# Performance work log

Measured on AMD Instinct MI355X. Metric: run time of the kernel, lower is better.

Reference implementation:

```python
import jax, jax.numpy as jnp
import numpy as np

B, N, T, H, F = 2, 1024, 12, 64, 1

def _diffuse(x, a):
    # x: (B,C,V), a: (B,W,V)  ->  (B,C,W)   (einsum 'ncvl,nwv->ncwl' with l=1)
    return jnp.einsum('bcv,bwv->bcw', x, a)

def _sconv(x, supports, order, include_self, W, b):
    feats = [x] if include_self else []
    for a in supports:
        x1 = _diffuse(x, a)
        feats.append(x1)
        for _ in range(order - 1):
            x1 = _diffuse(x1, a)
            feats.append(x1)
    z = jnp.concatenate(feats, axis=1)
    return jnp.einsum('bcn,oc->bon', z, W) + b[None, :, None]

def _lin(x, W, b):
    # Conv1d/Conv2d with kernel 1 == channel-wise linear
    return jnp.einsum('bcn,oc->bon', x, W) + b[None, :, None]

def setup_inputs():
    key = jax.random.key(0)
    ks = jax.random.split(key, 12)
    x = jax.random.normal(ks[0], (B, F, N, T), jnp.float32)
    mask = jax.random.randint(ks[1], (B, F, N, T), 0, 2, jnp.int32)
    adj = jax.random.uniform(ks[2], (2, B, N, N), jnp.float32)
    adj = adj / (adj.sum(-1, keepdims=True) + 1e-8)  # compute_support row-normalization
    cin_gate = 5 * (2 * F + H)  # (order*support_len+1)*(d_in+num_units) = 5*66
    s = 0.1
    Wr = s * jax.random.normal(ks[3], (H, cin_gate)); br = jnp.zeros((H,), jnp.float32)
    Wu = s * jax.random.normal(ks[4], (H, cin_gate)); bu = jnp.zeros((H,), jnp.float32)
    Wc = s * jax.random.normal(ks[5], (H, cin_gate)); bc = jnp.zeros((H,), jnp.float32)
    Wfs = s * jax.random.normal(ks[6], (F, H)); bfs = jnp.zeros((F,), jnp.float32)
    Wdin = s * jax.random.normal(ks[7], (H, 2 * F + H)); bdin = jnp.zeros((H,), jnp.float32)
    Wgc = s * jax.random.normal(ks[8], (H, 2 * H)); bgc = jnp.zeros((H,), jnp.float32)
    Wlout = s * jax.random.normal(ks[9], (H, 2 * H)); blout = jnp.zeros((H,), jnp.float32)
    Wro = s * jax.random.normal(ks[10], (F, 2 * H)); bro = jnp.zeros((F,), jnp.float32)
    prelu_a = 0.25 * jnp.ones((1,), jnp.float32)
    return dict(x=x, mask=mask, adj=adj, Wr=Wr, br=br, Wu=Wu, bu=bu, Wc=Wc, bc=bc,
                Wfs=Wfs, bfs=bfs, Wdin=Wdin, bdin=bdin, Wgc=Wgc, bgc=bgc,
                Wlout=Wlout, blout=blout, Wro=Wro, bro=bro, prelu_a=prelu_a)

def _gril(x, mask, adj, Wr, br, Wu, bu, Wc, bc, Wfs, bfs, Wdin, bdin,
          Wgc, bgc, Wlout, blout, Wro, bro, prelu_a):
    supports = [adj[0], adj[1]]
    h0 = jnp.zeros((x.shape[0], H, x.shape[2]), x.dtype)

    def step(h, inp):
        x_s, m_s = inp                  # (B,F,N), (B,F,N) int
        m_f = m_s.astype(x_s.dtype)
        m_b = m_s.astype(bool)
        # first stage prediction from hidden state
        xs1 = _lin(h, Wfs, bfs)
        x1 = jnp.where(m_b, x_s, xs1)
        # spatial decoder (order=1, no attention)
        x_in = _lin(jnp.concatenate([x1, m_f, h], axis=1), Wdin, bdin)
        out = _sconv(x_in, supports, 1, False, Wgc, bgc)
        out = _lin(jnp.concatenate([out, h], axis=1), Wlout, blout)
        out = jnp.where(out >= 0, out, prelu_a * out)   # PReLU
        repr_s = jnp.concatenate([out, h], axis=1)      # (B,2H,N)
        xs2 = _lin(repr_s, Wro, bro)
        x2 = jnp.where(m_b, x1, xs2)
        # GCGRU cell update (order=2 diffusion per gate)
        inp_c = jnp.concatenate([x2, m_f], axis=1)
        xh = jnp.concatenate([inp_c, h], axis=1)
        r = jax.nn.sigmoid(_sconv(xh, supports, 2, True, Wr, br))
        u = jax.nn.sigmoid(_sconv(xh, supports, 2, True, Wu, bu))
        xc = jnp.concatenate([inp_c, r * h], axis=1)
        c = jnp.tanh(_sconv(xc, supports, 2, True, Wc, bc))
        h_new = u * h + (1.0 - u) * c
        return h_new, (xs2, xs1, repr_s)

    xs = jnp.moveaxis(x, -1, 0)     # (T,B,F,N)
    ms = jnp.moveaxis(mask, -1, 0)
    _, (imps, preds, reprs) = jax.lax.scan(step, h0, (xs, ms))
    imputations = jnp.moveaxis(imps, 0, -1)       # (B,F,N,T)
    predictions = jnp.moveaxis(preds, 0, -1)      # (B,F,N,T)
    representations = jnp.moveaxis(reprs, 0, -1)  # (B,2H,N,T)
    return imputations, predictions, representations

def reference(x, mask, adj, Wr, br, Wu, bu, Wc, bc, Wfs, bfs, Wdin, bdin,
              Wgc, bgc, Wlout, blout, Wro, bro, prelu_a):
    return _gril(x, mask, adj, Wr, br, Wu, bu, Wc, bc, Wfs, bfs, Wdin, bdin,
                 Wgc, bgc, Wlout, blout, Wro, bro, prelu_a)
```

## Files before the change

### kernel.cpp

```cpp
#include <hip/hip_runtime.h>
#include <hip/hip_bf16.h>
#include <cstddef>

#define NN 1024
#define BB 2
#define TT 12
#define ZS 352

typedef __attribute__((ext_vector_type(8))) short short8;
typedef __attribute__((ext_vector_type(4))) short short4v;
typedef __attribute__((ext_vector_type(4))) float f32x4;
typedef __hip_bfloat16 bf16;

__device__ __forceinline__ float sigmoidf_(float v) { return 1.0f / (1.0f + expf(-v)); }
__device__ __forceinline__ short bf16s(float f) { bf16 h = __float2bfloat16(f); return *reinterpret_cast<short*>(&h); }

__device__ __forceinline__ float mapcol(const float* src, int c) {
    if (c < 64) return src[2 + c];
    if (c == 64) return src[0];
    if (c == 65) return src[1];
    if (c < 68 || c >= 340) return 0.f;
    const int d = c - 68, bk = d / 68, off = d % 68;
    if (off < 64) return src[66 + bk * 66 + 2 + off];
    if (off == 64) return src[66 + bk * 66];
    if (off == 65) return src[66 + bk * 66 + 1];
    return 0.f;
}

__global__ __launch_bounds__(256) void k_prep(
    const float* __restrict__ Wgc, const float* __restrict__ bgc,
    const float* __restrict__ Wdin, const float* __restrict__ bdin,
    const float* __restrict__ Wlout, const float* __restrict__ blout,
    const float* __restrict__ Wfs,
    const float* __restrict__ Wr, const float* __restrict__ Wu, const float* __restrict__ Wc,
    float* __restrict__ Wcomb, float* __restrict__ bcomb, float* __restrict__ blout2,
    bf16* __restrict__ Wpre, bf16* __restrict__ Wrub, bf16* __restrict__ Wcb)
{
    const int idx = blockIdx.x * 256 + threadIdx.x;
    if (idx < 8448) {
        const int o = idx / 66, k = idx % 66;
        const float* g = Wgc + (size_t)(o & 63) * 128 + (o >> 6) * 64;
        float a = 0.f;
#pragma unroll 8
        for (int c = 0; c < 64; ++c) a += g[c] * Wdin[c * 66 + k];
        Wcomb[idx] = a;
    } else if (idx < 8576) {
        const int o = idx - 8448;
        const float* g = Wgc + (size_t)(o & 63) * 128 + (o >> 6) * 64;
        float a = 0.f;
#pragma unroll 8
        for (int c = 0; c < 64; ++c) a += g[c] * bdin[c];
        bcomb[o] = a;
    } else if (idx < 8640) {
        const int oc = idx - 8576;
        float a = blout[oc];
#pragma unroll 8
        for (int j = 0; j < 64; ++j) a += Wlout[(size_t)oc * 128 + j] * bgc[j];
        blout2[oc] = a;
    } else if (idx < 17856) {
        const int j = idx - 8640, r = j >> 6, k = j & 63;
        float v = 0.f;
        if (r == 0) v = Wfs[k];
        else if (r <= 128) {
            const int o = r - 1;
            const float* g = Wgc + (size_t)(o & 63) * 128 + (o >> 6) * 64;
#pragma unroll 8
            for (int c = 0; c < 64; ++c) v += g[c] * Wdin[c * 66 + 2 + k];
        }
        Wpre[j] = __float2bfloat16(v);
    } else if (idx < 62912) {
        const int j = idx - 17856, r = j / 352, c = j % 352;
        const float* src = (r < 64) ? (Wr + (size_t)r * 330) : (Wu + (size_t)(r - 64) * 330);
        Wrub[j] = __float2bfloat16(mapcol(src, c));
    } else if (idx < 85440) {
        const int j = idx - 62912, r = j / 352, c = j % 352;
        Wcb[j] = __float2bfloat16(mapcol(Wc + (size_t)r * 330, c));
    }
}

__global__ __launch_bounds__(256) void k_cvtT(const float* __restrict__ adj,
                                              bf16* __restrict__ adjb, bf16* __restrict__ adjtb)
{
    const int sb = blockIdx.z;
    const int r0 = blockIdx.y * 64, c0 = blockIdx.x * 64;
    const float* A = adj + ((size_t)sb << 20);
    __shared__ short tile[64][72];
    const int tr = threadIdx.x >> 4, tc = (threadIdx.x & 15) * 4;
#pragma unroll
    for (int i = 0; i < 4; ++i) {
        const int r = tr + i * 16;
        float4 v = *reinterpret_cast<const float4*>(&A[(size_t)(r0 + r) * NN + c0 + tc]);
        short4v o = { bf16s(v.x), bf16s(v.y), bf16s(v.z), bf16s(v.w) };
        *reinterpret_cast<short4v*>(&adjb[((size_t)sb << 20) + (size_t)(r0 + r) * NN + c0 + tc]) = o;
        tile[r][tc + 0] = o.x; tile[r][tc + 1] = o.y; tile[r][tc + 2] = o.z; tile[r][tc + 3] = o.w;
    }
    __syncthreads();
#pragma unroll
    for (int i = 0; i < 4; ++i) {
        const int v = tr + i * 16;
        short4v o = { tile[tc + 0][v], tile[tc + 1][v], tile[tc + 2][v], tile[tc + 3][v] };
        *reinterpret_cast<short4v*>(&adjtb[((size_t)sb << 20) + (size_t)(c0 + v) * NN + r0 + tc]) = o;
    }
}

__global__ __launch_bounds__(256) void k_a2(const bf16* __restrict__ adjb,
                                            const bf16* __restrict__ adjtb,
                                            bf16* __restrict__ adj2b)
{
    const int sb = blockIdx.z;
    const int wave = threadIdx.x >> 6, lane = threadIdx.x & 63;
    const int lr = lane & 15, lq = lane >> 4;
    const int v0 = blockIdx.x * 64 + wave * 16;
    const int w0 = blockIdx.y * 64;
    const bf16* AT = adjtb + ((size_t)sb << 20) + (size_t)(v0 + lr) * NN + lq * 8;
    const bf16* Ar = adjb + ((size_t)sb << 20) + (size_t)(w0 + lr) * NN + lq * 8;
    f32x4 acc[4];
#pragma unroll
    for (int m = 0; m < 4; ++m) acc[m] = (f32x4){0.f, 0.f, 0.f, 0.f};
#pragma unroll 4
    for (int k0 = 0; k0 < NN; k0 += 32) {
        short8 bfr = *reinterpret_cast<const short8*>(AT + k0);
        short8 af[4];
#pragma unroll
        for (int m = 0; m < 4; ++m)
            af[m] = *reinterpret_cast<const short8*>(Ar + (size_t)m * 16 * NN + k0);
#pragma unroll
        for (int m = 0; m < 4; ++m)
            acc[m] = __builtin_amdgcn_mfma_f32_16x16x32_bf16(af[m], bfr, acc[m], 0, 0, 0);
    }
    bf16* D = adj2b + ((size_t)sb << 20);
#pragma unroll
    for (int m = 0; m < 4; ++m)
#pragma unroll
        for (int q = 0; q < 4; ++q)
            D[(size_t)(w0 + m * 16 + lq * 4 + q) * NN + v0 + lr] = __float2bfloat16(acc[m][q]);
}

__global__ __launch_bounds__(64) void k_pre(
    const bf16* __restrict__ Wpre, const bf16* __restrict__ zT,
    const float* __restrict__ Wcomb, const float* __restrict__ bcomb,
    const float* __restrict__ bfsp,
    const float* __restrict__ x, const int* __restrict__ mask,
    bf16* __restrict__ yb, float* __restrict__ x1b, float* __restrict__ pred, int t)
{
    const int lane = threadIdx.x & 63, lr = lane & 15, lq = lane >> 4;
    const int p = blockIdx.x * 16 + lr;
    const bf16* B = zT + (size_t)p * ZS;
    f32x4 acc[9];
#pragma unroll
    for (int m = 0; m < 9; ++m) acc[m] = (f32x4){0.f, 0.f, 0.f, 0.f};
#pragma unroll
    for (int ks = 0; ks < 2; ++ks) {
        short8 bfr = *reinterpret_cast<const short8*>(B + ks * 32 + lq * 8);
#pragma unroll
        for (int m = 0; m < 9; ++m) {
            short8 af = *reinterpret_cast<const short8*>(Wpre + (size_t)(m * 16 + lr) * 64 + ks * 32 + lq * 8);
            acc[m] = __builtin_amdgcn_mfma_f32_16x16x32_bf16(af, bfr, acc[m], 0, 0, 0);
        }
    }
    const int b = p >> 10, n = p & (NN - 1);
    const size_t xi = (size_t)p * TT + t;
    const float xs1v = acc[0][0] + bfsp[0];
    const float xs1 = __shfl(xs1v, lr);
    const int mi = mask[xi];
    const float mf = (float)mi;
    const float x1 = mi ? x[xi] : xs1;
    if (lq == 0) { pred[xi] = xs1; x1b[p] = x1; }
#pragma unroll
    for (int m = 0; m < 9; ++m)
#pragma unroll
        for (int q = 0; q < 4; ++q) {
            const int o = m * 16 + lq * 4 + q - 1;
            if (o >= 0 && o < 128) {
                const float val = acc[m][q] + Wcomb[o * 66] * x1 + Wcomb[o * 66 + 1] * mf + bcomb[o];
                yb[(size_t)(b * 128 + o) * NN + n] = __float2bfloat16(val);
            }
        }
}

__global__ __launch_bounds__(256) void k_difN(
    int mode, const bf16* __restrict__ adjb, const bf16* __restrict__ adj2b,
    const bf16* __restrict__ yb, const bf16* __restrict__ zb, const bf16* __restrict__ zcb,
    float* __restrict__ gcT, bf16* __restrict__ zT, bf16* __restrict__ zcT)
{
    const int combo = blockIdx.y;
    const int wave = threadIdx.x >> 6, lane = threadIdx.x & 63;
    const int lr = lane & 15, lq = lane >> 4;
    const int n0 = blockIdx.x * 32;

    int s, b, ord; const bf16* X; bool toGc = false;
    if (mode == 0 && combo < 4) {
        s = combo >> 1; b = combo & 1; ord = 0; toGc = true;
        X = yb + ((size_t)(b * 128 + s * 64)) * NN;
    } else {
        const int i = (mode == 0) ? combo - 4 : combo;
        b = i & 1; s = (i >> 1) & 1; ord = i >> 2;
        X = ((mode == 0) ? zb : zcb) + ((size_t)b * 66) * NN;
    }
    const int sb = s * 2 + b;
    const bf16* M = (ord ? adj2b : adjb) + ((size_t)sb << 20);
    const bf16* A = M + (size_t)(n0 + lr) * NN + lq * 8;
    const bf16* Xp = X + (size_t)lr * NN + lq * 8;

    f32x4 acc[2][4];
#pragma unroll
    for (int nt = 0; nt < 2; ++nt)
#pragma unroll
        for (int m = 0; m < 4; ++m) acc[nt][m] = (f32x4){0.f, 0.f, 0.f, 0.f};
    const int vbeg = wave * 256;
#pragma unroll 2
    for (int i = 0; i < 8; ++i) {
        const int v0 = vbeg + i * 32;
        short8 bfr[2], af[4];
#pragma unroll
        for (int nt = 0; nt < 2; ++nt)
            bfr[nt] = *reinterpret_cast<const short8*>(A + (size_t)nt * 16 * NN + v0);
#pragma unroll
        for (int m = 0; m < 4; ++m)
            af[m] = *reinterpret_cast<const short8*>(Xp + (size_t)m * 16 * NN + v0);
#pragma unroll
        for (int nt = 0; nt < 2; ++nt)
#pragma unroll
            for (int m = 0; m < 4; ++m)
                acc[nt][m] = __builtin_amdgcn_mfma_f32_16x16x32_bf16(af[m], bfr[nt], acc[nt][m], 0, 0, 0);
    }
    __shared__ f32x4 red[3][2][4][64];
    if (wave > 0) {
#pragma unroll
        for (int nt = 0; nt < 2; ++nt)
#pragma unroll
            for (int m = 0; m < 4; ++m) red[wave - 1][nt][m][lane] = acc[nt][m];
    }
    __syncthreads();
    if (wave == 0) {
#pragma unroll
        for (int nt = 0; nt < 2; ++nt) {
#pragma unroll
            for (int m = 0; m < 4; ++m)
                acc[nt][m] += red[0][nt][m][lane] + red[1][nt][m][lane] + red[2][nt][m][lane];
            const int p = b * NN + n0 + nt * 16 + lr;
            if (toGc) {
#pragma unroll
                for (int m = 0; m < 4; ++m)
                    *reinterpret_cast<f32x4*>(&gcT[(size_t)p * 128 + s * 64 + m * 16 + lq * 4]) = acc[nt][m];
            } else {
                bf16* dst = ((mode == 0) ? zT : zcT) + (size_t)p * ZS + 68 + (s * 2 + ord) * 68;
#pragma unroll
                for (int m = 0; m < 4; ++m) {
                    short4v o = { bf16s(acc[nt][m][0]), bf16s(acc[nt][m][1]),
                                  bf16s(acc[nt][m][2]), bf16s(acc[nt][m][3]) };
                    *reinterpret_cast<short4v*>(dst + m * 16 + lq * 4) = o;
                }
            }
        }
    }
}

__global__ __launch_bounds__(256) void k_dif2(
    const bf16* __restrict__ adjb, const bf16* __restrict__ adj2b,
    const bf16* __restrict__ zb, bf16* __restrict__ zT, bf16* __restrict__ zcT)
{
    const int i = blockIdx.y;
    const int b = i & 1, s = (i >> 1) & 1, ord = i >> 2;
    const int sb = s * 2 + b;
    const int wave = threadIdx.x >> 6, lane = threadIdx.x & 63;
    const int lr = lane & 15, lq = lane >> 4;
    const int n0 = blockIdx.x * 16;
    const bf16* M = (ord ? adj2b : adjb) + ((size_t)sb << 20);
    const bf16* A = M + (size_t)(n0 + lr) * NN + lq * 8;
    const bf16* Xp = zb + ((size_t)(b * 66 + 64) + lr) * NN + lq * 8;

    f32x4 acc = (f32x4){0.f, 0.f, 0.f, 0.f};
    const short8 zsh = {0, 0, 0, 0, 0, 0, 0, 0};
    const int vbeg = wave * 256;
#pragma unroll 4
    for (int i2 = 0; i2 < 8; ++i2) {
        const int v0 = vbeg + i2 * 32;
        short8 bfr = *reinterpret_cast<const short8*>(A + v0);
        short8 af = (lr < 2) ? *reinterpret_cast<const short8*>(Xp + v0) : zsh;
        acc = __builtin_amdgcn_mfma_f32_16x16x32_bf16(af, bfr, acc, 0, 0, 0);
    }
    __shared__ f32x4 red2[3][64];
    if (wave > 0) red2[wave - 1][lane] = acc;
    __syncthreads();
    if (wave == 0 && lq == 0) {
        acc += red2[0][lane] + red2[1][lane] + red2[2][lane];
        const int p = b * NN + n0 + lr;
        const size_t off = (size_t)p * ZS + 68 + (s * 2 + ord) * 68 + 64;
#pragma unroll
        for (int q = 0; q < 2; ++q) {
            const bf16 v = __float2bfloat16(acc[q]);
            zT[off + q] = v; zcT[off + q] = v;
        }
    }
}

__global__ __launch_bounds__(256) void k_stepB(
    const float* __restrict__ gcT, const float* __restrict__ hTf,
    const float* __restrict__ Wlout, const float* __restrict__ blout2,
    const float* __restrict__ prelu_a, const float* __restrict__ Wro,
    const float* __restrict__ bro, const float* __restrict__ x1b,
    const int* __restrict__ mask,
    float* __restrict__ imp, float* __restrict__ repr,
    bf16* __restrict__ zb, bf16* __restrict__ zcb,
    bf16* __restrict__ zT, bf16* __restrict__ zcT, int t)
{
    const int wv = threadIdx.x >> 6, lane = threadIdx.x & 63;
    const int p = blockIdx.x * 4 + wv;
    const int b = p >> 10, n = p & (NN - 1);
    __shared__ float gl[4][64], hl[4][64];
    const float g = gcT[(size_t)p * 128 + lane] + gcT[(size_t)p * 128 + 64 + lane];
    const float hv = hTf[(size_t)p * 64 + lane];
    gl[wv][lane] = g;
    hl[wv][lane] = hv;
    __syncthreads();
    const float* w = Wlout + (size_t)lane * 128;
    float a = 0.f;
#pragma unroll 8
    for (int j = 0; j < 64; ++j)
        a += w[j] * gl[wv][j] + w[64 + j] * hl[wv][j];
    float v = a + blout2[lane];
    v = (v >= 0.f) ? v : prelu_a[0] * v;
    repr[(((size_t)b * 128 + lane) * NN + n) * TT + t] = v;
    repr[(((size_t)b * 128 + 64 + lane) * NN + n) * TT + t] = hv;
    float s = Wro[lane] * v + Wro[64 + lane] * hv;
#pragma unroll
    for (int off = 32; off > 0; off >>= 1) s += __shfl_xor(s, off);
    if (lane == 0) {
        const float xs2 = s + bro[0];
        const size_t xi = (size_t)p * TT + t;
        imp[xi] = xs2;
        const int mi = mask[xi];
        const float x2 = mi ? x1b[p] : xs2;
        const bf16 x2b = __float2bfloat16(x2);
        const bf16 mb = __float2bfloat16((float)mi);
        zb[((size_t)b * 66 + 64) * NN + n] = x2b;
        zb[((size_t)b * 66 + 65) * NN + n] = mb;
        zcb[((size_t)b * 66 + 64) * NN + n] = x2b;
        zcb[((size_t)b * 66 + 65) * NN + n] = mb;
        zT[(size_t)p * ZS + 64] = x2b; zT[(size_t)p * ZS + 65] = mb;
        zcT[(size_t)p * ZS + 64] = x2b; zcT[(size_t)p * ZS + 65] = mb;
    }
}

__global__ __launch_bounds__(128) void k_gates(
    const bf16* __restrict__ Wrub, const bf16* __restrict__ zT,
    const float* __restrict__ br, const float* __restrict__ bu,
    const float* __restrict__ hTf,
    float* __restrict__ uT, bf16* __restrict__ zcb, bf16* __restrict__ zcT)
{
    const int wave = threadIdx.x >> 6, lane = threadIdx.x & 63;
    const int lr = lane & 15, lq = lane >> 4;
    const int p = blockIdx.x * 16 + lr;
    const bf16* B = zT + (size_t)p * ZS;
    const bf16* WA = Wrub + (size_t)wave * 64 * ZS;
    f32x4 acc[4];
#pragma unroll
    for (int m = 0; m < 4; ++m) acc[m] = (f32x4){0.f, 0.f, 0.f, 0.f};
#pragma unroll 2
    for (int ks = 0; ks < 11; ++ks) {
        short8 bfr = *reinterpret_cast<const short8*>(B + ks * 32 + lq * 8);
#pragma unroll
        for (int m = 0; m < 4; ++m) {
            short8 af = *reinterpret_cast<const short8*>(WA + (size_t)(m * 16 + lr) * ZS + ks * 32 + lq * 8);
            acc[m] = __builtin_amdgcn_mfma_f32_16x16x32_bf16(af, bfr, acc[m], 0, 0, 0);
        }
    }
    const int b = p >> 10, n = p & (NN - 1);
    if (wave == 0) {
#pragma unroll
        for (int m = 0; m < 4; ++m) {
            short4v rq;
#pragma unroll
            for (int q = 0; q < 4; ++q) {
                const int oc = m * 16 + lq * 4 + q;
                const float rv = sigmoidf_(acc[m][q] + br[oc]);
                const float rh = rv * hTf[(size_t)p * 64 + oc];
                rq[q] = bf16s(rh);
                zcb[((size_t)b * 66 + oc) * NN + n] = __float2bfloat16(rh);
            }
            *reinterpret_cast<short4v*>(&zcT[(size_t)p * ZS + m * 16 + lq * 4]) = rq;
        }
    } else {
#pragma unroll
        for (int m = 0; m < 4; ++m) {
            f32x4 uq;
#pragma unroll
            for (int q = 0; q < 4; ++q) {
                const int oc = m * 16 + lq * 4 + q;
                uq[q] = sigmoidf_(acc[m][q] + bu[oc]);
            }
            *reinterpret_cast<f32x4*>(&uT[(size_t)p * 64 + m * 16 + lq * 4]) = uq;
        }
    }
}

__global__ __launch_bounds__(128) void k_cellpre(
    const bf16* __restrict__ Wcb, const bf16* __restrict__ zcT,
    const float* __restrict__ bc, const float* __restrict__ uT,
    float* __restrict__ hTf, bf16* __restrict__ zT, bf16* __restrict__ zb,
    const bf16* __restrict__ Wpre, const float* __restrict__ Wcomb,
    const float* __restrict__ bcomb, const float* __restrict__ bfsp,
    const float* __restrict__ x, const int* __restrict__ mask,
    bf16* __restrict__ yb, float* __restrict__ x1b, float* __restrict__ pred, int tn)
{
    const int wave = threadIdx.x >> 6, lane = threadIdx.x & 63;
    const int lr = lane & 15, lq = lane >> 4;
    const int p = blockIdx.x * 16 + lr;
    const int b = p >> 10, n = p & (NN - 1);
    __shared__ short hsm[16][72];
    __shared__ float xs1s[16];

    {
        const bf16* B = zcT + (size_t)p * ZS;
        f32x4 acc[2];
#pragma unroll
        for (int mm = 0; mm < 2; ++mm) acc[mm] = (f32x4){0.f, 0.f, 0.f, 0.f};
#pragma unroll 2
        for (int ks = 0; ks < 11; ++ks) {
            short8 bfr = *reinterpret_cast<const short8*>(B + ks * 32 + lq * 8);
#pragma unroll
            for (int mm = 0; mm < 2; ++mm) {
                const int m = wave * 2 + mm;
                short8 af = *reinterpret_cast<const short8*>(Wcb + (size_t)(m * 16 + lr) * ZS + ks * 32 + lq * 8);
                acc[mm] = __builtin_amdgcn_mfma_f32_16x16x32_bf16(af, bfr, acc[mm], 0, 0, 0);
            }
        }
#pragma unroll
        for (int mm = 0; mm < 2; ++mm) {
            const int m = wave * 2 + mm;
            f32x4 hq;
            short4v hb;
#pragma unroll
            for (int q = 0; q < 4; ++q) {
                const int oc = m * 16 + lq * 4 + q;
                const float cv = tanhf(acc[mm][q] + bc[oc]);
                const float uv = uT[(size_t)p * 64 + oc];
                const float ho = hTf[(size_t)p * 64 + oc];
                const float hn = uv * ho + (1.f - uv) * cv;
                hq[q] = hn;
                hb[q] = bf16s(hn);
                zb[((size_t)b * 66 + oc) * NN + n] = __float2bfloat16(hn);
            }
            *reinterpret_cast<f32x4*>(&hTf[(size_t)p * 64 + m * 16 + lq * 4]) = hq;
            *reinterpret_cast<short4v*>(&zT[(size_t)p * ZS + m * 16 + lq * 4]) = hb;
            *reinterpret_cast<short4v*>(&hsm[lr][m * 16 + lq * 4]) = hb;
        }
    }
    __syncthreads();

    {
        const int MB = wave ? 4 : 5;
        f32x4 acc[5];
#pragma unroll
        for (int m = 0; m < 5; ++m) acc[m] = (f32x4){0.f, 0.f, 0.f, 0.f};
#pragma unroll
        for (int ks = 0; ks < 2; ++ks) {
            short8 bfr = *reinterpret_cast<const short8*>(&hsm[lr][ks * 32 + lq * 8]);
#pragma unroll
            for (int m = 0; m < 5; ++m) {
                if (m < MB) {
                    const int mm = wave ? 5 + m : m;
                    short8 af = *reinterpret_cast<const short8*>(Wpre + (size_t)(mm * 16 + lr) * 64 + ks * 32 + lq * 8);
                    acc[m] = __builtin_amdgcn_mfma_f32_16x16x32_bf16(af, bfr, acc[m], 0, 0, 0);
                }
            }
        }
        if (wave == 0 && lq == 0) xs1s[lr] = acc[0][0] + bfsp[0];
        __syncthreads();
        const float xs1 = xs1s[lr];
        const size_t xi = (size_t)p * TT + tn;
        const int mi = mask[xi];
        const float mf = (float)mi;
        const float x1 = mi ? x[xi] : xs1;
        if (wave == 0 && lq == 0) { pred[xi] = xs1; x1b[p] = x1; }
#pragma unroll
        for (int m = 0; m < 5; ++m) {
            if (m < MB) {
                const int mm = wave ? 5 + m : m;
#pragma unroll
                for (int q = 0; q < 4; ++q) {
                    const int o = mm * 16 + lq * 4 + q - 1;
                    if (o >= 0 && o < 128) {
                        const float val = acc[m][q] + Wcomb[o * 66] * x1 + Wcomb[o * 66 + 1] * mf + bcomb[o];
                        yb[(size_t)(b * 128 + o) * NN + n] = __float2bfloat16(val);
                    }
                }
            }
        }
    }
}

extern "C" void kernel_launch(void* const* d_in, const int* in_sizes, int n_in,
                              void* d_out, int out_size, void* d_ws, size_t ws_size,
                              hipStream_t stream)
{
    const float* x     = (const float*)d_in[0];
    const int*   mask  = (const int*)  d_in[1];
    const float* adj   = (const float*)d_in[2];
    const float* Wr    = (const float*)d_in[3];
    const float* br    = (const float*)d_in[4];
    const float* Wu    = (const float*)d_in[5];
    const float* bu    = (const float*)d_in[6];
    const float* Wc    = (const float*)d_in[7];
    const float* bc    = (const float*)d_in[8];
    const float* Wfs   = (const float*)d_in[9];
    const float* bfs   = (const float*)d_in[10];
    const float* Wdin  = (const float*)d_in[11];
    const float* bdin  = (const float*)d_in[12];
    const float* Wgc   = (const float*)d_in[13];
    const float* bgc   = (const float*)d_in[14];
    const float* Wlout = (const float*)d_in[15];
    const float* blout = (const float*)d_in[16];
    const float* Wro   = (const float*)d_in[17];
    const float* bro   = (const float*)d_in[18];
    const float* pa    = (const float*)d_in[19];

    float* ws = (float*)d_ws;
    float* Wcomb  = ws + 0;
    float* bcomb  = ws + 8448;
    float* blout2 = ws + 8576;
    float* x1b    = ws + 8640;
    float* gcT    = ws + 10688;
    float* uT     = ws + 272832;
    float* hTf    = ws + 403904;
    bf16* bfp   = (bf16*)(ws + 534976);
    bf16* zb    = bfp + 0;
    bf16* zcb   = bfp + 135168;
    bf16* zT    = bfp + 270336;
    bf16* zcT   = bfp + 991232;
    bf16* adjb  = bfp + 1712128;
    bf16* adjtb = bfp + 5906432;
    bf16* adj2b = bfp + 10100736;
    bf16* yb    = bfp + 14295040;
    bf16* Wpre  = bfp + 14557184;
    bf16* Wrub  = bfp + 14566400;
    bf16* Wcb   = bfp + 14611456;

    float* imp  = (float*)d_out;
    float* pred = imp + (size_t)BB * NN * TT;
    float* repr = imp + (size_t)2 * BB * NN * TT;

    hipMemsetAsync(hTf, 0, 131072 * 4 + (size_t)1712128 * 2, stream);
    hipLaunchKernelGGL(k_prep, dim3(334), dim3(256), 0, stream,
                       Wgc, bgc, Wdin, bdin, Wlout, blout, Wfs, Wr, Wu, Wc,
                       Wcomb, bcomb, blout2, Wpre, Wrub, Wcb);
    hipLaunchKernelGGL(k_cvtT, dim3(16, 16, 4), dim3(256), 0, stream, adj, adjb, adjtb);
    hipLaunchKernelGGL(k_a2, dim3(16, 16, 4), dim3(256), 0, stream, adjb, adjtb, adj2b);

    hipLaunchKernelGGL(k_pre, dim3(128), dim3(64), 0, stream,
                       Wpre, zT, Wcomb, bcomb, bfs, x, mask, yb, x1b, pred, 0);

    for (int t = 0; t < TT; ++t) {
        const int ncombo = (t < TT - 1) ? 12 : 4;
        hipLaunchKernelGGL(k_difN, dim3(32, ncombo), dim3(256), 0, stream,
                           0, adjb, adj2b, yb, zb, zcb, gcT, zT, zcT);
        hipLaunchKernelGGL(k_stepB, dim3(512), dim3(256), 0, stream,
                           gcT, hTf, Wlout, blout2, pa, Wro, bro, x1b, mask,
                           imp, repr, zb, zcb, zT, zcT, t);
        if (t < TT - 1) {
            hipLaunchKernelGGL(k_dif2, dim3(64, 8), dim3(256), 0, stream,
                               adjb, adj2b, zb, zT, zcT);
            hipLaunchKernelGGL(k_gates, dim3(128), dim3(128), 0, stream,
                               Wrub, zT, br, bu, hTf, uT, zcb, zcT);
            hipLaunchKernelGGL(k_difN, dim3(32, 8), dim3(256), 0, stream,
                               1, adjb, adj2b, yb, zb, zcb, gcT, zT, zcT);
            hipLaunchKernelGGL(k_cellpre, dim3(128), dim3(128), 0, stream,
                               Wcb, zcT, bc, uT, hTf, zT, zb,
                               Wpre, Wcomb, bcomb, bfs, x, mask, yb, x1b, pred, t + 1);
        }
    }
}
```

Baseline: 765.2 us.

## Fuse output-readout stage into graph-diffusion kernel and retile adjacency-square GEMM

```diff
diff --git a/kernel.cpp b/kernel.cpp
--- a/kernel.cpp
+++ b/kernel.cpp
@@ -34,7 +34,8 @@
     const float* __restrict__ Wfs,
     const float* __restrict__ Wr, const float* __restrict__ Wu, const float* __restrict__ Wc,
     float* __restrict__ Wcomb, float* __restrict__ bcomb, float* __restrict__ blout2,
-    bf16* __restrict__ Wpre, bf16* __restrict__ Wrub, bf16* __restrict__ Wcb)
+    bf16* __restrict__ Wpre, bf16* __restrict__ Wrub, bf16* __restrict__ Wcb,
+    bf16* __restrict__ Wlb)
 {
     const int idx = blockIdx.x * 256 + threadIdx.x;
     if (idx < 8448) {
@@ -75,6 +76,9 @@
     } else if (idx < 85440) {
         const int j = idx - 62912, r = j / 352, c = j % 352;
         Wcb[j] = __float2bfloat16(mapcol(Wc + (size_t)r * 330, c));
+    } else if (idx < 93632) {
+        const int j = idx - 85440;
+        Wlb[j] = __float2bfloat16(Wlout[j]);
     }
 }
 
@@ -110,30 +114,38 @@
     const int sb = blockIdx.z;
     const int wave = threadIdx.x >> 6, lane = threadIdx.x & 63;
     const int lr = lane & 15, lq = lane >> 4;
-    const int v0 = blockIdx.x * 64 + wave * 16;
+    const int v0 = blockIdx.x * 128 + wave * 32;
     const int w0 = blockIdx.y * 64;
     const bf16* AT = adjtb + ((size_t)sb << 20) + (size_t)(v0 + lr) * NN + lq * 8;
     const bf16* Ar = adjb + ((size_t)sb << 20) + (size_t)(w0 + lr) * NN + lq * 8;
-    f32x4 acc[4];
-#pragma unroll
-    for (int m = 0; m < 4; ++m) acc[m] = (f32x4){0.f, 0.f, 0.f, 0.f};
-#pragma unroll 4
+    f32x4 acc[4][2];
+#pragma unroll
+    for (int m = 0; m < 4; ++m)
+#pragma unroll
+        for (int nb = 0; nb < 2; ++nb) acc[m][nb] = (f32x4){0.f, 0.f, 0.f, 0.f};
+#pragma unroll 2
     for (int k0 = 0; k0 < NN; k0 += 32) {
-        short8 bfr = *reinterpret_cast<const short8*>(AT + k0);
-        short8 af[4];
+        short8 bfr[2], af[4];
+#pragma unroll
+        for (int nb = 0; nb < 2; ++nb)
+            bfr[nb] = *reinterpret_cast<const short8*>(AT + (size_t)nb * 16 * NN + k0);
 #pragma unroll
         for (int m = 0; m < 4; ++m)
             af[m] = *reinterpret_cast<const short8*>(Ar + (size_t)m * 16 * NN + k0);
 #pragma unroll
         for (int m = 0; m < 4; ++m)
-            acc[m] = __builtin_amdgcn_mfma_f32_16x16x32_bf16(af[m], bfr, acc[m], 0, 0, 0);
+#pragma unroll
+            for (int nb = 0; nb < 2; ++nb)
+                acc[m][nb] = __builtin_amdgcn_mfma_f32_16x16x32_bf16(af[m], bfr[nb], acc[m][nb], 0, 0, 0);
     }
     bf16* D = adj2b + ((size_t)sb << 20);
 #pragma unroll
     for (int m = 0; m < 4; ++m)
 #pragma unroll
-        for (int q = 0; q < 4; ++q)
-            D[(size_t)(w0 + m * 16 + lq * 4 + q) * NN + v0 + lr] = __float2bfloat16(acc[m][q]);
+        for (int nb = 0; nb < 2; ++nb)
+#pragma unroll
+            for (int q = 0; q < 4; ++q)
+                D[(size_t)(w0 + m * 16 + lq * 4 + q) * NN + v0 + nb * 16 + lr] = __float2bfloat16(acc[m][nb][q]);
 }
 
 __global__ __launch_bounds__(64) void k_pre(
@@ -141,7 +153,7 @@
     const float* __restrict__ Wcomb, const float* __restrict__ bcomb,
     const float* __restrict__ bfsp,
     const float* __restrict__ x, const int* __restrict__ mask,
-    bf16* __restrict__ yb, float* __restrict__ x1b, float* __restrict__ pred, int t)
+    bf16* __restrict__ yb, float* __restrict__ pred, int t)
 {
     const int lane = threadIdx.x & 63, lr = lane & 15, lq = lane >> 4;
     const int p = blockIdx.x * 16 + lr;
@@ -165,7 +177,7 @@
     const int mi = mask[xi];
     const float mf = (float)mi;
     const float x1 = mi ? x[xi] : xs1;
-    if (lq == 0) { pred[xi] = xs1; x1b[p] = x1; }
+    if (lq == 0) pred[xi] = xs1;
 #pragma unroll
     for (int m = 0; m < 9; ++m)
 #pragma unroll
@@ -178,79 +190,261 @@
         }
 }
 
-__global__ __launch_bounds__(256) void k_difN(
-    int mode, const bf16* __restrict__ adjb, const bf16* __restrict__ adj2b,
-    const bf16* __restrict__ yb, const bf16* __restrict__ zb, const bf16* __restrict__ zcb,
-    float* __restrict__ gcT, bf16* __restrict__ zT, bf16* __restrict__ zcT)
-{
-    const int combo = blockIdx.y;
+__global__ __launch_bounds__(256) void k_difA(
+    const bf16* __restrict__ adjb, const bf16* __restrict__ adj2b,
+    const bf16* __restrict__ yb, const bf16* __restrict__ zbi,
+    const bf16* __restrict__ Wlb, const float* __restrict__ blout2,
+    const float* __restrict__ prelu_a, const float* __restrict__ Wro,
+    const float* __restrict__ bro, const float* __restrict__ x,
+    const int* __restrict__ mask, const float* __restrict__ hTf,
+    float* __restrict__ imp, float* __restrict__ repr,
+    bf16* __restrict__ zb, bf16* __restrict__ zcb,
+    bf16* __restrict__ zT, bf16* __restrict__ zcT, int t)
+{
     const int wave = threadIdx.x >> 6, lane = threadIdx.x & 63;
     const int lr = lane & 15, lq = lane >> 4;
     const int n0 = blockIdx.x * 32;
 
-    int s, b, ord; const bf16* X; bool toGc = false;
-    if (mode == 0 && combo < 4) {
-        s = combo >> 1; b = combo & 1; ord = 0; toGc = true;
-        X = yb + ((size_t)(b * 128 + s * 64)) * NN;
-    } else {
-        const int i = (mode == 0) ? combo - 4 : combo;
-        b = i & 1; s = (i >> 1) & 1; ord = i >> 2;
-        X = ((mode == 0) ? zb : zcb) + ((size_t)b * 66) * NN;
-    }
-    const int sb = s * 2 + b;
-    const bf16* M = (ord ? adj2b : adjb) + ((size_t)sb << 20);
-    const bf16* A = M + (size_t)(n0 + lr) * NN + lq * 8;
-    const bf16* Xp = X + (size_t)lr * NN + lq * 8;
-
-    f32x4 acc[2][4];
-#pragma unroll
-    for (int nt = 0; nt < 2; ++nt)
-#pragma unroll
-        for (int m = 0; m < 4; ++m) acc[nt][m] = (f32x4){0.f, 0.f, 0.f, 0.f};
-    const int vbeg = wave * 256;
+    __shared__ f32x4 red[3][2][2][4][64];
+    __shared__ short gh[32][136];
+    __shared__ float hf[32][68];
+    __shared__ float lo_sm[32][68];
+
+    if (blockIdx.y >= 2) {
+        const int i = blockIdx.y - 2;
+        const int b = i & 1, s = (i >> 1) & 1, ord = i >> 2;
+        const int sb = s * 2 + b;
+        const bf16* M = (ord ? adj2b : adjb) + ((size_t)sb << 20);
+        const bf16* A = M + (size_t)(n0 + lr) * NN + lq * 8;
+        const bf16* Xp = zbi + ((size_t)(b * 66 + lr)) * NN + lq * 8;
+        f32x4 acc[2][4];
+#pragma unroll
+        for (int nt = 0; nt < 2; ++nt)
+#pragma unroll
+            for (int m = 0; m < 4; ++m) acc[nt][m] = (f32x4){0.f, 0.f, 0.f, 0.f};
+        const int vbeg = wave * 256;
 #pragma unroll 2
-    for (int i = 0; i < 8; ++i) {
-        const int v0 = vbeg + i * 32;
-        short8 bfr[2], af[4];
-#pragma unroll
-        for (int nt = 0; nt < 2; ++nt)
-            bfr[nt] = *reinterpret_cast<const short8*>(A + (size_t)nt * 16 * NN + v0);
-#pragma unroll
-        for (int m = 0; m < 4; ++m)
-            af[m] = *reinterpret_cast<const short8*>(Xp + (size_t)m * 16 * NN + v0);
-#pragma unroll
-        for (int nt = 0; nt < 2; ++nt)
+        for (int it = 0; it < 8; ++it) {
+            const int v0 = vbeg + it * 32;
+            short8 bfr[2], af[4];
+#pragma unroll
+            for (int nt = 0; nt < 2; ++nt)
+                bfr[nt] = *reinterpret_cast<const short8*>(A + (size_t)nt * 16 * NN + v0);
 #pragma unroll
             for (int m = 0; m < 4; ++m)
-                acc[nt][m] = __builtin_amdgcn_mfma_f32_16x16x32_bf16(af[m], bfr[nt], acc[nt][m], 0, 0, 0);
-    }
-    __shared__ f32x4 red[3][2][4][64];
-    if (wave > 0) {
-#pragma unroll
-        for (int nt = 0; nt < 2; ++nt)
-#pragma unroll
-            for (int m = 0; m < 4; ++m) red[wave - 1][nt][m][lane] = acc[nt][m];
-    }
-    __syncthreads();
-    if (wave == 0) {
-#pragma unroll
-        for (int nt = 0; nt < 2; ++nt) {
-#pragma unroll
-            for (int m = 0; m < 4; ++m)
-                acc[nt][m] += red[0][nt][m][lane] + red[1][nt][m][lane] + red[2][nt][m][lane];
-            const int p = b * NN + n0 + nt * 16 + lr;
-            if (toGc) {
+                af[m] = *reinterpret_cast<const short8*>(Xp + (size_t)m * 16 * NN + v0);
+#pragma unroll
+            for (int nt = 0; nt < 2; ++nt)
 #pragma unroll
                 for (int m = 0; m < 4; ++m)
-                    *reinterpret_cast<f32x4*>(&gcT[(size_t)p * 128 + s * 64 + m * 16 + lq * 4]) = acc[nt][m];
-            } else {
-                bf16* dst = ((mode == 0) ? zT : zcT) + (size_t)p * ZS + 68 + (s * 2 + ord) * 68;
+                    acc[nt][m] = __builtin_amdgcn_mfma_f32_16x16x32_bf16(af[m], bfr[nt], acc[nt][m], 0, 0, 0);
+        }
+        if (wave > 0) {
+#pragma unroll
+            for (int nt = 0; nt < 2; ++nt)
+#pragma unroll
+                for (int m = 0; m < 4; ++m) red[wave - 1][0][nt][m][lane] = acc[nt][m];
+        }
+        __syncthreads();
+        if (wave == 0) {
+#pragma unroll
+            for (int nt = 0; nt < 2; ++nt) {
+#pragma unroll
+                for (int m = 0; m < 4; ++m)
+                    acc[nt][m] += red[0][0][nt][m][lane] + red[1][0][nt][m][lane] + red[2][0][nt][m][lane];
+                const int p = b * NN + n0 + nt * 16 + lr;
+                bf16* dst = zT + (size_t)p * ZS + 68 + (s * 2 + ord) * 68;
 #pragma unroll
                 for (int m = 0; m < 4; ++m) {
                     short4v o = { bf16s(acc[nt][m][0]), bf16s(acc[nt][m][1]),
                                   bf16s(acc[nt][m][2]), bf16s(acc[nt][m][3]) };
                     *reinterpret_cast<short4v*>(dst + m * 16 + lq * 4) = o;
                 }
+            }
+        }
+        return;
+    }
+
+    const int b = blockIdx.y;
+    f32x4 acc[2][2][4];
+#pragma unroll
+    for (int s = 0; s < 2; ++s)
+#pragma unroll
+        for (int nt = 0; nt < 2; ++nt)
+#pragma unroll
+            for (int m = 0; m < 4; ++m) acc[s][nt][m] = (f32x4){0.f, 0.f, 0.f, 0.f};
+    {
+        const int vbeg = wave * 256;
+#pragma unroll 2
+        for (int it = 0; it < 8; ++it) {
+            const int v0 = vbeg + it * 32;
+            short8 bfr[2][2], af[2][4];
+#pragma unroll
+            for (int s = 0; s < 2; ++s) {
+                const bf16* M = adjb + ((size_t)(s * 2 + b) << 20);
+#pragma unroll
+                for (int nt = 0; nt < 2; ++nt)
+                    bfr[s][nt] = *reinterpret_cast<const short8*>(M + (size_t)(n0 + nt * 16 + lr) * NN + v0 + lq * 8);
+#pragma unroll
+                for (int m = 0; m < 4; ++m)
+                    af[s][m] = *reinterpret_cast<const short8*>(yb + (size_t)(b * 128 + s * 64 + m * 16 + lr) * NN + v0 + lq * 8);
+            }
+#pragma unroll
+            for (int s = 0; s < 2; ++s)
+#pragma unroll
+                for (int nt = 0; nt < 2; ++nt)
+#pragma unroll
+                    for (int m = 0; m < 4; ++m)
+                        acc[s][nt][m] = __builtin_amdgcn_mfma_f32_16x16x32_bf16(af[s][m], bfr[s][nt], acc[s][nt][m], 0, 0, 0);
+        }
+    }
+    if (wave > 0) {
+#pragma unroll
+        for (int s = 0; s < 2; ++s)
+#pragma unroll
+            for (int nt = 0; nt < 2; ++nt)
+#pragma unroll
+                for (int m = 0; m < 4; ++m) red[wave - 1][s][nt][m][lane] = acc[s][nt][m];
+    }
+    if (wave == 1 || wave == 2) {
+        const int nb = (wave - 1) * 16;
+        for (int i = lane; i < 1024; i += 64) {
+            const int node = nb + (i >> 6), oc = i & 63;
+            const float hv = hTf[(size_t)(b * NN + n0 + node) * 64 + oc];
+            hf[node][oc] = hv;
+            gh[node][64 + oc] = bf16s(hv);
+            repr[(((size_t)b * 128 + 64 + oc) * NN + (n0 + node)) * TT + t] = hv;
+        }
+    }
+    __syncthreads();
+    if (wave == 0) {
+#pragma unroll
+        for (int nt = 0; nt < 2; ++nt) {
+#pragma unroll
+            for (int m = 0; m < 4; ++m) {
+                f32x4 g = acc[0][nt][m] + acc[1][nt][m];
+#pragma unroll
+                for (int w = 0; w < 3; ++w) g += red[w][0][nt][m][lane] + red[w][1][nt][m][lane];
+                const int node = nt * 16 + lr;
+#pragma unroll
+                for (int q = 0; q < 4; ++q) gh[node][m * 16 + lq * 4 + q] = bf16s(g[q]);
+            }
+        }
+    }
+    __syncthreads();
+    {
+        f32x4 dacc[2];
+#pragma unroll
+        for (int nt = 0; nt < 2; ++nt) dacc[nt] = (f32x4){0.f, 0.f, 0.f, 0.f};
+#pragma unroll
+        for (int ks = 0; ks < 4; ++ks) {
+            short8 af = *reinterpret_cast<const short8*>(Wlb + (size_t)(wave * 16 + lr) * 128 + ks * 32 + lq * 8);
+#pragma unroll
+            for (int nt = 0; nt < 2; ++nt) {
+                short8 bfr = *reinterpret_cast<const short8*>(&gh[nt * 16 + lr][ks * 32 + lq * 8]);
+                dacc[nt] = __builtin_amdgcn_mfma_f32_16x16x32_bf16(af, bfr, dacc[nt], 0, 0, 0);
+            }
+        }
+        const float pa = prelu_a[0];
+#pragma unroll
+        for (int nt = 0; nt < 2; ++nt) {
+            const int node = nt * 16 + lr;
+#pragma unroll
+            for (int q = 0; q < 4; ++q) {
+                const int oc = wave * 16 + lq * 4 + q;
+                float v = dacc[nt][q] + blout2[oc];
+                v = (v >= 0.f) ? v : pa * v;
+                repr[(((size_t)b * 128 + oc) * NN + (n0 + node)) * TT + t] = v;
+                lo_sm[node][oc] = v;
+            }
+        }
+    }
+    __syncthreads();
+    {
+        const int node = threadIdx.x >> 3, sub = threadIdx.x & 7;
+        float s = 0.f;
+#pragma unroll
+        for (int j = sub * 8; j < sub * 8 + 8; ++j)
+            s += Wro[j] * lo_sm[node][j] + Wro[64 + j] * hf[node][j];
+        s += __shfl_xor(s, 1); s += __shfl_xor(s, 2); s += __shfl_xor(s, 4);
+        if (sub == 0) {
+            const float xs2 = s + bro[0];
+            const int n = n0 + node;
+            const int p = b * NN + n;
+            const size_t xi = (size_t)p * TT + t;
+            imp[xi] = xs2;
+            const int mi = mask[xi];
+            const float x2 = mi ? x[xi] : xs2;
+            const bf16 x2b = __float2bfloat16(x2);
+            const bf16 mb = __float2bfloat16((float)mi);
+            zb[((size_t)b * 66 + 64) * NN + n] = x2b;
+            zb[((size_t)b * 66 + 65) * NN + n] = mb;
+            zcb[((size_t)b * 66 + 64) * NN + n] = x2b;
+            zcb[((size_t)b * 66 + 65) * NN + n] = mb;
+            zT[(size_t)p * ZS + 64] = x2b; zT[(size_t)p * ZS + 65] = mb;
+            zcT[(size_t)p * ZS + 64] = x2b; zcT[(size_t)p * ZS + 65] = mb;
+        }
+    }
+}
+
+__global__ __launch_bounds__(256) void k_difN(
+    const bf16* __restrict__ adjb, const bf16* __restrict__ adj2b,
+    const bf16* __restrict__ zcb, float* __restrict__ gcT_unused,
+    bf16* __restrict__ zcT)
+{
+    const int i = blockIdx.y;
+    const int b = i & 1, s = (i >> 1) & 1, ord = i >> 2;
+    const int wave = threadIdx.x >> 6, lane = threadIdx.x & 63;
+    const int lr = lane & 15, lq = lane >> 4;
+    const int n0 = blockIdx.x * 32;
+    const int sb = s * 2 + b;
+    const bf16* M = (ord ? adj2b : adjb) + ((size_t)sb << 20);
+    const bf16* A = M + (size_t)(n0 + lr) * NN + lq * 8;
+    const bf16* Xp = zcb + ((size_t)(b * 66 + lr)) * NN + lq * 8;
+
+    f32x4 acc[2][4];
+#pragma unroll
+    for (int nt = 0; nt < 2; ++nt)
+#pragma unroll
+        for (int m = 0; m < 4; ++m) acc[nt][m] = (f32x4){0.f, 0.f, 0.f, 0.f};
+    const int vbeg = wave * 256;
+#pragma unroll 2
+    for (int it = 0; it < 8; ++it) {
+        const int v0 = vbeg + it * 32;
+        short8 bfr[2], af[4];
+#pragma unroll
+        for (int nt = 0; nt < 2; ++nt)
+            bfr[nt] = *reinterpret_cast<const short8*>(A + (size_t)nt * 16 * NN + v0);
+#pragma unroll
+        for (int m = 0; m < 4; ++m)
+            af[m] = *reinterpret_cast<const short8*>(Xp + (size_t)m * 16 * NN + v0);
+#pragma unroll
+        for (int nt = 0; nt < 2; ++nt)
+#pragma unroll
+            for (int m = 0; m < 4; ++m)
+                acc[nt][m] = __builtin_amdgcn_mfma_f32_16x16x32_bf16(af[m], bfr[nt], acc[nt][m], 0, 0, 0);
+    }
+    __shared__ f32x4 red[3][2][4][64];
+    if (wave > 0) {
+#pragma unroll
+        for (int nt = 0; nt < 2; ++nt)
+#pragma unroll
+            for (int m = 0; m < 4; ++m) red[wave - 1][nt][m][lane] = acc[nt][m];
+    }
+    __syncthreads();
+    if (wave == 0) {
+#pragma unroll
+        for (int nt = 0; nt < 2; ++nt) {
+#pragma unroll
+            for (int m = 0; m < 4; ++m)
+                acc[nt][m] += red[0][nt][m][lane] + red[1][nt][m][lane] + red[2][nt][m][lane];
+            const int p = b * NN + n0 + nt * 16 + lr;
+            bf16* dst = zcT + (size_t)p * ZS + 68 + (s * 2 + ord) * 68;
+#pragma unroll
+            for (int m = 0; m < 4; ++m) {
+                short4v o = { bf16s(acc[nt][m][0]), bf16s(acc[nt][m][1]),
+                              bf16s(acc[nt][m][2]), bf16s(acc[nt][m][3]) };
+                *reinterpret_cast<short4v*>(dst + m * 16 + lq * 4) = o;
             }
         }
     }
@@ -295,54 +489,6 @@
     }
 }
 
-__global__ __launch_bounds__(256) void k_stepB(
-    const float* __restrict__ gcT, const float* __restrict__ hTf,
-    const float* __restrict__ Wlout, const float* __restrict__ blout2,
-    const float* __restrict__ prelu_a, const float* __restrict__ Wro,
-    const float* __restrict__ bro, const float* __restrict__ x1b,
-    const int* __restrict__ mask,
-    float* __restrict__ imp, float* __restrict__ repr,
-    bf16* __restrict__ zb, bf16* __restrict__ zcb,
-    bf16* __restrict__ zT, bf16* __restrict__ zcT, int t)
-{
-    const int wv = threadIdx.x >> 6, lane = threadIdx.x & 63;
-    const int p = blockIdx.x * 4 + wv;
-    const int b = p >> 10, n = p & (NN - 1);
-    __shared__ float gl[4][64], hl[4][64];
-    const float g = gcT[(size_t)p * 128 + lane] + gcT[(size_t)p * 128 + 64 + lane];
-    const float hv = hTf[(size_t)p * 64 + lane];
-    gl[wv][lane] = g;
-    hl[wv][lane] = hv;
-    __syncthreads();
-    const float* w = Wlout + (size_t)lane * 128;
-    float a = 0.f;
-#pragma unroll 8
-    for (int j = 0; j < 64; ++j)
-        a += w[j] * gl[wv][j] + w[64 + j] * hl[wv][j];
-    float v = a + blout2[lane];
-    v = (v >= 0.f) ? v : prelu_a[0] * v;
-    repr[(((size_t)b * 128 + lane) * NN + n) * TT + t] = v;
-    repr[(((size_t)b * 128 + 64 + lane) * NN + n) * TT + t] = hv;
-    float s = Wro[lane] * v + Wro[64 + lane] * hv;
-#pragma unroll
-    for (int off = 32; off > 0; off >>= 1) s += __shfl_xor(s, off);
-    if (lane == 0) {
-        const float xs2 = s + bro[0];
-        const size_t xi = (size_t)p * TT + t;
-        imp[xi] = xs2;
-        const int mi = mask[xi];
-        const float x2 = mi ? x1b[p] : xs2;
-        const bf16 x2b = __float2bfloat16(x2);
-        const bf16 mb = __float2bfloat16((float)mi);
-        zb[((size_t)b * 66 + 64) * NN + n] = x2b;
-        zb[((size_t)b * 66 + 65) * NN + n] = mb;
-        zcb[((size_t)b * 66 + 64) * NN + n] = x2b;
-        zcb[((size_t)b * 66 + 65) * NN + n] = mb;
-        zT[(size_t)p * ZS + 64] = x2b; zT[(size_t)p * ZS + 65] = mb;
-        zcT[(size_t)p * ZS + 64] = x2b; zcT[(size_t)p * ZS + 65] = mb;
-    }
-}
-
 __global__ __launch_bounds__(128) void k_gates(
     const bf16* __restrict__ Wrub, const bf16* __restrict__ zT,
     const float* __restrict__ br, const float* __restrict__ bu,
@@ -402,7 +548,7 @@
     const bf16* __restrict__ Wpre, const float* __restrict__ Wcomb,
     const float* __restrict__ bcomb, const float* __restrict__ bfsp,
     const float* __restrict__ x, const int* __restrict__ mask,
-    bf16* __restrict__ yb, float* __restrict__ x1b, float* __restrict__ pred, int tn)
+    bf16* __restrict__ yb, float* __restrict__ pred, int tn)
 {
     const int wave = threadIdx.x >> 6, lane = threadIdx.x & 63;
     const int lr = lane & 15, lq = lane >> 4;
@@ -473,7 +619,7 @@
         const int mi = mask[xi];
         const float mf = (float)mi;
         const float x1 = mi ? x[xi] : xs1;
-        if (wave == 0 && lq == 0) { pred[xi] = xs1; x1b[p] = x1; }
+        if (wave == 0 && lq == 0) pred[xi] = xs1;
 #pragma unroll
         for (int m = 0; m < 5; ++m) {
             if (m < MB) {
@@ -520,8 +666,6 @@
     float* Wcomb  = ws + 0;
     float* bcomb  = ws + 8448;
     float* blout2 = ws + 8576;
-    float* x1b    = ws + 8640;
-    float* gcT    = ws + 10688;
     float* uT     = ws + 272832;
     float* hTf    = ws + 403904;
     bf16* bfp   = (bf16*)(ws + 534976);
@@ -536,38 +680,37 @@
     bf16* Wpre  = bfp + 14557184;
     bf16* Wrub  = bfp + 14566400;
     bf16* Wcb   = bfp + 14611456;
+    bf16* Wlb   = bfp + 14633984;
 
     float* imp  = (float*)d_out;
     float* pred = imp + (size_t)BB * NN * TT;
     float* repr = imp + (size_t)2 * BB * NN * TT;
 
     hipMemsetAsync(hTf, 0, 131072 * 4 + (size_t)1712128 * 2, stream);
-    hipLaunchKernelGGL(k_prep, dim3(334), dim3(256), 0, stream,
+    hipLaunchKernelGGL(k_prep, dim3(366), dim3(256), 0, stream,
                        Wgc, bgc, Wdin, bdin, Wlout, blout, Wfs, Wr, Wu, Wc,
-                       Wcomb, bcomb, blout2, Wpre, Wrub, Wcb);
+                       Wcomb, bcomb, blout2, Wpre, Wrub, Wcb, Wlb);
     hipLaunchKernelGGL(k_cvtT, dim3(16, 16, 4), dim3(256), 0, stream, adj, adjb, adjtb);
-    hipLaunchKernelGGL(k_a2, dim3(16, 16, 4), dim3(256), 0, stream, adjb, adjtb, adj2b);
+    hipLaunchKernelGGL(k_a2, dim3(8, 16, 4), dim3(256), 0, stream, adjb, adjtb, adj2b);
 
     hipLaunchKernelGGL(k_pre, dim3(128), dim3(64), 0, stream,
-                       Wpre, zT, Wcomb, bcomb, bfs, x, mask, yb, x1b, pred, 0);
+                       Wpre, zT, Wcomb, bcomb, bfs, x, mask, yb, pred, 0);
 
     for (int t = 0; t < TT; ++t) {
-        const int ncombo = (t < TT - 1) ? 12 : 4;
-        hipLaunchKernelGGL(k_difN, dim3(32, ncombo), dim3(256), 0, stream,
-                           0, adjb, adj2b, yb, zb, zcb, gcT, zT, zcT);
-        hipLaunchKernelGGL(k_stepB, dim3(512), dim3(256), 0, stream,
-                           gcT, hTf, Wlout, blout2, pa, Wro, bro, x1b, mask,
-                           imp, repr, zb, zcb, zT, zcT, t);
+        const int ny = (t < TT - 1) ? 10 : 2;
+        hipLaunchKernelGGL(k_difA, dim3(32, ny), dim3(256), 0, stream,
+                           adjb, adj2b, yb, zb, Wlb, blout2, pa, Wro, bro, x, mask,
+                           hTf, imp, repr, zb, zcb, zT, zcT, t);
         if (t < TT - 1) {
             hipLaunchKernelGGL(k_dif2, dim3(64, 8), dim3(256), 0, stream,
                                adjb, adj2b, zb, zT, zcT);
             hipLaunchKernelGGL(k_gates, dim3(128), dim3(128), 0, stream,
                                Wrub, zT, br, bu, hTf, uT, zcb, zcT);
             hipLaunchKernelGGL(k_difN, dim3(32, 8), dim3(256), 0, stream,
-                               1, adjb, adj2b, yb, zb, zcb, gcT, zT, zcT);
+                               adjb, adj2b, zcb, (float*)nullptr, zcT);
             hipLaunchKernelGGL(k_cellpre, dim3(128), dim3(128), 0, stream,
                                Wcb, zcT, bc, uT, hTf, zT, zb,
-                               Wpre, Wcomb, bcomb, bfs, x, mask, yb, x1b, pred, t + 1);
-        }
-    }
-}
+                               Wpre, Wcomb, bcomb, bfs, x, mask, yb, pred, t + 1);
+        }
+    }
+}
```

New measurement: 705.0 us. -7.9%, faster.
